# Optimization experiments

Hardware: AMD Instinct MI355X
Metric: run time of the kernel (lower is better)

## Reference

```python
import jax, jax.numpy as jnp
import numpy as np

RES = 32
HEADS = 16
EMB = 1024
DIM_HEAD = EMB // HEADS
BATCH = 8
N = RES * RES
SCALE = DIM_HEAD ** -0.5


def _make_bias_idxs():
    # replicate the LeViT-style |dx|,|dy| offset indexing from __init__
    points = [(i, j) for i in range(RES) for j in range(RES)]
    offsets = {}
    idxs = []
    for p1 in points:
        for p2 in points:
            off = (abs(p1[0] - p2[0]), abs(p1[1] - p2[1]))
            if off not in offsets:
                offsets[off] = len(offsets)
            idxs.append(offsets[off])
    return np.asarray(idxs, dtype=np.int32).reshape(N, N), len(offsets)


def setup_inputs() -> dict:
    key = jax.random.key(0)
    k_x, k_qkv, k_b, k_o = jax.random.split(key, 4)
    bias_idxs, n_off = _make_bias_idxs()  # n_off == 1024 for a 32x32 grid
    return {
        "x": jax.random.normal(k_x, (BATCH, N, EMB), dtype=jnp.float32),
        "W_qkv": jax.random.normal(k_qkv, (3 * EMB, EMB), dtype=jnp.float32) * 0.02,
        "attention_biases": jax.random.normal(k_b, (HEADS, n_off), dtype=jnp.float32) * 0.02,
        "bias_idxs": jnp.asarray(bias_idxs),
        "W_out": jax.random.normal(k_o, (EMB, EMB), dtype=jnp.float32) * 0.02,
        "b_out": jnp.zeros((EMB,), dtype=jnp.float32),
    }


def reference(x, W_qkv, attention_biases, bias_idxs, W_out, b_out):
    B, n, E = x.shape
    # to_qkv: Linear(E, 3E, bias=False) -> x @ W^T
    qkv = x @ W_qkv.T  # [B, n, 3E]
    q, k, v = jnp.split(qkv, 3, axis=-1)

    def heads(t):  # b n (h d) -> b h n d
        return t.reshape(B, n, HEADS, DIM_HEAD).transpose(0, 2, 1, 3)

    q, k, v = heads(q), heads(k), heads(v)
    qk = jnp.einsum("bhnd,bhmd->bhnm", q, k) * SCALE  # [B, h, n, n]
    bias = attention_biases[:, bias_idxs]  # gather -> [h, n, n]
    qk = qk + bias[None]
    attn = jax.nn.softmax(qk, axis=-1)
    out = jnp.einsum("bhnm,bhmd->bhnd", attn, v)
    out = out.transpose(0, 2, 1, 3).reshape(B, n, E)  # b h n d -> b n (h d)
    # to_out: Linear(E, E) with bias (dropout p=0 is identity)
    return out @ W_out.T + b_out
```

## Files before the change

### kernel.cpp

```cpp
#include <hip/hip_runtime.h>

typedef __attribute__((ext_vector_type(8))) short bf16x8;
typedef __attribute__((ext_vector_type(4))) short bf16x4;
typedef __attribute__((ext_vector_type(4))) float f32x4;

#define L2E 1.44269504088896340736f
#define QSCL 0.18033688011112042f

__device__ inline unsigned short f2bf(float f) {
  union { float f; unsigned int u; } x; x.f = f;
  return (unsigned short)((x.u + 0x8000u) >> 16);
}
__device__ inline unsigned int f2bf2(float a, float b) {
  union { float f; unsigned int u; } xa, xb;
  xa.f = a; xb.f = b;
  return ((xa.u + 0x8000u) >> 16) | (((xb.u + 0x8000u) & 0xFFFF0000u));
}
__device__ inline unsigned int pk_bf16(float a, float b) {
#if __has_builtin(__builtin_amdgcn_cvt_pk_bf16_f32)
  typedef __attribute__((ext_vector_type(2))) __bf16 bfv2;
  union { bfv2 v; unsigned int u; } x;
  x.v = __builtin_amdgcn_cvt_pk_bf16_f32(a, b);
  return x.u;
#else
  return f2bf2(a, b);
#endif
}

__device__ inline void gl_lds16(const void* g, void* l) {
  __builtin_amdgcn_global_load_lds((const __attribute__((address_space(1))) void*)g,
                                   (__attribute__((address_space(3))) void*)l,
                                   16, 0, 0);
}

__device__ inline void vm_drain() {
  asm volatile("s_waitcnt vmcnt(0)" ::: "memory");
}
__device__ inline void vm_wait4() {
  asm volatile("s_waitcnt vmcnt(4)" ::: "memory");
}
__device__ inline void vm_wait3() {
  asm volatile("s_waitcnt vmcnt(3)" ::: "memory");
}

#define N4_X  2097152
#define N4_WQ 786432
#define N4_WO 262144
__global__ void cast3_kernel(const float* __restrict__ x,
                             const float* __restrict__ wq,
                             const float* __restrict__ wo,
                             unsigned short* __restrict__ xb,
                             unsigned short* __restrict__ wqb,
                             unsigned short* __restrict__ wob) {
  int i = blockIdx.x * blockDim.x + threadIdx.x;
  int st = gridDim.x * blockDim.x;
  for (; i < N4_X + N4_WQ + N4_WO; i += st) {
    const float* src; unsigned short* dst; int j;
    if (i < N4_X)            { src = x;  dst = xb;  j = i; }
    else if (i < N4_X + N4_WQ){ src = wq; dst = wqb; j = i - N4_X; }
    else                     { src = wo; dst = wob; j = i - N4_X - N4_WQ; }
    float4 v = reinterpret_cast<const float4*>(src)[j];
    ushort4 o;
    o.x = f2bf(v.x); o.y = f2bf(v.y); o.z = f2bf(v.z); o.w = f2bf(v.w);
    reinterpret_cast<ushort4*>(dst)[j] = o;
  }
}

template <int MODE>
__device__ __forceinline__ void gemm_qkv_body(
    unsigned short* __restrict__ sA,
    unsigned short* __restrict__ sB,
    const unsigned short* __restrict__ A,
    const unsigned short* __restrict__ Bm,
    unsigned short* __restrict__ qo,
    unsigned short* __restrict__ ko,
    unsigned short* __restrict__ vo) {
  const int K = 1024;
  const int tid = threadIdx.x;
  const int w = tid >> 6, lane = tid & 63;
  const int l15 = lane & 15, quad = lane >> 4;
  const int wm = (w >> 1) * 64, wn = (w & 1) * 64;
  const int tm = blockIdx.y, tn = blockIdx.x;

  const unsigned short* Ab = A + (size_t)(tm * 128) * K;
  const unsigned short* Bb = Bm + (size_t)(tn * 128) * K;

  const int srow = w * 32 + (lane >> 2);
  const int scol = (((lane & 3) ^ ((lane >> 3) & 3))) * 8;
  const int rsw = (l15 >> 1) & 3;

  const f32x4 fz = {0.f, 0.f, 0.f, 0.f};
  f32x4 acc[4][4];
#pragma unroll
  for (int i = 0; i < 4; i++)
#pragma unroll
    for (int j = 0; j < 4; j++) acc[i][j] = fz;

#define QKV_STAGE(kn, nb)                                                        \
  do {                                                                           \
    gl_lds16(Ab + (size_t)srow * K + (kn) + scol,        &sA[(nb) * 4096 + (w * 32) * 32]);      \
    gl_lds16(Ab + (size_t)(srow + 16) * K + (kn) + scol, &sA[(nb) * 4096 + (w * 32 + 16) * 32]); \
    gl_lds16(Bb + (size_t)srow * K + (kn) + scol,        &sB[(nb) * 4096 + (w * 32) * 32]);      \
    gl_lds16(Bb + (size_t)(srow + 16) * K + (kn) + scol, &sB[(nb) * 4096 + (w * 32 + 16) * 32]); \
  } while (0)

  QKV_STAGE(0, 0);
  QKV_STAGE(32, 1);

  int bi = 0;
  for (int k0 = 0; k0 < K; k0 += 32) {
    if (k0 + 64 < K) vm_wait4(); else vm_drain();
    __syncthreads();
    if (k0 + 64 < K) {
      int nb = bi + 2; if (nb >= 3) nb -= 3;
      QKV_STAGE(k0 + 64, nb);
    }
    bf16x8 af[4], bfr[4];
#pragma unroll
    for (int mt = 0; mt < 4; mt++)
      af[mt] = *(const bf16x8*)&sA[bi * 4096 + (wm + mt * 16 + l15) * 32 + ((quad ^ rsw) << 3)];
#pragma unroll
    for (int nt = 0; nt < 4; nt++)
      bfr[nt] = *(const bf16x8*)&sB[bi * 4096 + (wn + nt * 16 + l15) * 32 + ((quad ^ rsw) << 3)];
#pragma unroll
    for (int mt = 0; mt < 4; mt++)
#pragma unroll
      for (int nt = 0; nt < 4; nt++) {
        if (MODE == 0)
          acc[mt][nt] = __builtin_amdgcn_mfma_f32_16x16x32_bf16(bfr[nt], af[mt], acc[mt][nt], 0, 0, 0);
        else
          acc[mt][nt] = __builtin_amdgcn_mfma_f32_16x16x32_bf16(af[mt], bfr[nt], acc[mt][nt], 0, 0, 0);
      }
    bi = bi + 1; if (bi == 3) bi = 0;
  }
#undef QKV_STAGE

  const int m0 = tm * 128;
  const int bb = m0 >> 10, n0 = m0 & 1023;
  const int cbase = (tn * 128) & 1023;

  if (MODE == 0) {
    const int which = tn >> 3;
    const float scl = (which == 0) ? QSCL : 1.0f;
    unsigned short* dst = (which == 0) ? qo : ko;
#pragma unroll
    for (int mt = 0; mt < 4; mt++) {
      int tok = n0 + wm + mt * 16 + l15;
#pragma unroll
      for (int nt = 0; nt < 4; nt++) {
        int c = cbase + wn + nt * 16 + quad * 4;
        int hh = c >> 6, d0 = c & 63;
        uint2 val;
        val.x = f2bf2(acc[mt][nt][0] * scl, acc[mt][nt][1] * scl);
        val.y = f2bf2(acc[mt][nt][2] * scl, acc[mt][nt][3] * scl);
        *(uint2*)&dst[(((size_t)bb * 16 + hh) * 1024 + tok) * 64 + d0] = val;
      }
    }
  } else {
#pragma unroll
    for (int mt = 0; mt < 4; mt++) {
      int tok = n0 + wm + mt * 16 + quad * 4;
#pragma unroll
      for (int nt = 0; nt < 4; nt++) {
        int c = cbase + wn + nt * 16 + l15;
        int hh = c >> 6, dd = c & 63;
        uint2 val;
        val.x = f2bf2(acc[mt][nt][0], acc[mt][nt][1]);
        val.y = f2bf2(acc[mt][nt][2], acc[mt][nt][3]);
        *(uint2*)&vo[(((size_t)bb * 16 + hh) * 64 + dd) * 1024 + tok] = val;
      }
    }
  }
}

__global__ __launch_bounds__(256, 3) void gemm_qkv(
    const unsigned short* __restrict__ A,
    const unsigned short* __restrict__ Bm,
    unsigned short* __restrict__ qo,
    unsigned short* __restrict__ ko,
    unsigned short* __restrict__ vo) {
  __shared__ unsigned short sA[3][128 * 32];
  __shared__ unsigned short sB[3][128 * 32];
  if (blockIdx.x < 16) gemm_qkv_body<0>(&sA[0][0], &sB[0][0], A, Bm, qo, ko, vo);
  else                 gemm_qkv_body<1>(&sA[0][0], &sB[0][0], A, Bm, qo, ko, vo);
}

__global__ __launch_bounds__(256, 2) void attn_kernel(
    const unsigned short* __restrict__ Q,
    const unsigned short* __restrict__ Kg,
    const unsigned short* __restrict__ Vt,
    const float* __restrict__ biases,
    unsigned short* __restrict__ Og) {
  __shared__ unsigned short sK[2][64 * 64];
  __shared__ unsigned short sV[2][64 * 64];
  __shared__ float sBias2[32 * 63];

  const int bx = blockIdx.x;
  const int bh = bx & 127, qt = bx >> 7;
  const int h = bh & 15, b = bh >> 4;
  const int tid = threadIdx.x, w = tid >> 6, lane = tid & 63;
  const int l15 = lane & 15, quad = lane >> 4;

  const size_t bhs = (size_t)(b * 16 + h);
  const unsigned short* qbase = Q + (bhs * 1024 + (size_t)qt * 256) * 64;
  const unsigned short* kbase = Kg + bhs * 1024 * 64;
  const unsigned short* vbase = Vt + bhs * 64 * 1024;

  for (int t = tid; t < 2048; t += 256) {
    int d = t >> 6, u = t & 63;
    if (u < 63) {
      int dj = u - 31; dj = dj < 0 ? -dj : dj;
      sBias2[d * 63 + u] = biases[h * 1024 + d * 32 + dj] * L2E;
    }
  }

  const int sr0 = w * 16 + (lane >> 3);
  const int sc8 = lane & 7;
  const int sw0 = sc8 ^ (lane >> 3);

  gl_lds16(kbase + (size_t)sr0 * 64 + sw0 * 8,        &sK[0][(w * 16) * 64]);
  gl_lds16(kbase + (size_t)(sr0 + 8) * 64 + sw0 * 8,  &sK[0][(w * 16 + 8) * 64]);
  gl_lds16(vbase + (size_t)sr0 * 1024 + sw0 * 8,      &sV[0][(w * 16) * 64]);
  gl_lds16(vbase + (size_t)(sr0 + 8) * 1024 + sw0 * 8,&sV[0][(w * 16 + 8) * 64]);

  bf16x8 qf[4][2];
#pragma unroll
  for (int qb = 0; qb < 4; qb++)
#pragma unroll
    for (int kd = 0; kd < 2; kd++)
      qf[qb][kd] = *(const bf16x8*)(qbase + (w * 64 + qb * 16 + l15) * 64 + kd * 32 + quad * 8);

  const int qg0 = qt * 256 + w * 64;
  const int qtw = __builtin_amdgcn_readfirstlane(qt * 8 + w * 2);
  int cc2[2][2];
#pragma unroll
  for (int qh = 0; qh < 2; qh++)
#pragma unroll
    for (int kp = 0; kp < 2; kp++)
      cc2[qh][kp] = qh * 16 + l15 - kp * 16 - quad * 4;

  const f32x4 fz = {0.f, 0.f, 0.f, 0.f};
  f32x4 of[4][4], osum[4];
#pragma unroll
  for (int i = 0; i < 4; i++) {
    osum[i] = fz;
#pragma unroll
    for (int j = 0; j < 4; j++) of[i][j] = fz;
  }
  const bf16x4 vones = {(short)0x3F80, (short)0x3F80, (short)0x3F80, (short)0x3F80};

  int buf = 0;
  for (int j0 = 0; j0 < 1024; j0 += 64) {
    vm_drain();
    __syncthreads();
    if (j0 + 64 < 1024) {
      int nb = buf ^ 1, jn = j0 + 64;
      gl_lds16(kbase + (size_t)(jn + sr0) * 64 + sw0 * 8,       &sK[nb][(w * 16) * 64]);
      gl_lds16(kbase + (size_t)(jn + sr0 + 8) * 64 + sw0 * 8,   &sK[nb][(w * 16 + 8) * 64]);
      gl_lds16(vbase + (size_t)sr0 * 1024 + jn + sw0 * 8,       &sV[nb][(w * 16) * 64]);
      gl_lds16(vbase + (size_t)(sr0 + 8) * 1024 + jn + sw0 * 8, &sV[nb][(w * 16 + 8) * 64]);
    }
    const unsigned short* K_ = sK[buf];
    const unsigned short* V_ = sV[buf];
    const int j5 = j0 >> 5;
    const int dh = qtw - j5;
    const float* b0 = sBias2 + abs(dh) * 63 + 31;
    const float* bM = sBias2 + abs(dh - 1) * 63 + 31;
    const float* bP = sBias2 + abs(dh + 1) * 63 + 31;

#pragma unroll
    for (int kvb = 0; kvb < 4; kvb++) {
      bf16x8 kf0 = *(const bf16x8*)&K_[(kvb * 16 + l15) * 64 + ((quad ^ (l15 & 7)) << 3)];
      bf16x8 kf1 = *(const bf16x8*)&K_[(kvb * 16 + l15) * 64 + (((4 + quad) ^ (l15 & 7)) << 3)];
      bf16x4 vf[4];
#pragma unroll
      for (int nt = 0; nt < 4; nt++) {
        int d = nt * 16 + l15;
        vf[nt] = *(const bf16x4*)&V_[d * 64 + (((kvb * 2 + (quad >> 1)) ^ (l15 & 7)) << 3) + (quad & 1) * 4];
      }
      const int kp = kvb & 1;
#pragma unroll
      for (int qb = 0; qb < 4; qb++) {
        f32x4 s4 = __builtin_amdgcn_mfma_f32_16x16x32_bf16(kf0, qf[qb][0], fz, 0, 0, 0);
        s4 = __builtin_amdgcn_mfma_f32_16x16x32_bf16(kf1, qf[qb][1], s4, 0, 0, 0);
        const float* bp = (qb < 2) ? ((kvb < 2) ? b0 : bM)
                                   : ((kvb < 2) ? bP : b0);
        const float* bq = bp + cc2[qb & 1][kp];
        float p0 = __builtin_amdgcn_exp2f(s4.x + bq[0]);
        float p1 = __builtin_amdgcn_exp2f(s4.y + bq[-1]);
        float p2 = __builtin_amdgcn_exp2f(s4.z + bq[-2]);
        float p3 = __builtin_amdgcn_exp2f(s4.w + bq[-3]);
        union { unsigned int u[2]; bf16x4 v; } pk;
        pk.u[0] = pk_bf16(p0, p1);
        pk.u[1] = pk_bf16(p2, p3);
#pragma unroll
        for (int nt = 0; nt < 4; nt++)
          of[qb][nt] = __builtin_amdgcn_mfma_f32_16x16x16bf16_1k(pk.v, vf[nt], of[qb][nt], 0, 0, 0);
        osum[qb] = __builtin_amdgcn_mfma_f32_16x16x16bf16_1k(pk.v, vones, osum[qb], 0, 0, 0);
      }
    }
    buf ^= 1;
  }

  const int kvq = quad * 4;
#pragma unroll
  for (int qb = 0; qb < 4; qb++)
#pragma unroll
    for (int r = 0; r < 4; r++) {
      float inv = __builtin_amdgcn_rcpf(osum[qb][r]);
      int n = qg0 + qb * 16 + kvq + r;
      size_t orow = ((size_t)b * 1024 + n) * 1024 + h * 64;
#pragma unroll
      for (int nt = 0; nt < 4; nt++)
        Og[orow + nt * 16 + l15] = f2bf(of[qb][nt][r] * inv);
    }
}

__global__ __launch_bounds__(256, 4) void gemm_out_k(
    const unsigned short* __restrict__ A,
    const unsigned short* __restrict__ Bm,
    const float* __restrict__ bias,
    float* __restrict__ out) {
  __shared__ unsigned short sA[3][128 * 32];
  __shared__ unsigned short sB[3][64 * 32];
  const int K = 1024;
  const int tid = threadIdx.x;
  const int w = tid >> 6, lane = tid & 63;
  const int l15 = lane & 15, quad = lane >> 4;
  const int tm = blockIdx.y, tn = blockIdx.x;

  const unsigned short* Ab = A + (size_t)(tm * 128) * K;
  const unsigned short* Bb = Bm + (size_t)(tn * 64) * K;

  const int srowA = w * 32 + (lane >> 2);
  const int srowB = w * 16 + (lane >> 2);
  const int scol = (((lane & 3) ^ ((lane >> 3) & 3))) * 8;
  const int rsw = (l15 >> 1) & 3;

  const f32x4 fz = {0.f, 0.f, 0.f, 0.f};
  f32x4 acc[2][4];
#pragma unroll
  for (int i = 0; i < 2; i++)
#pragma unroll
    for (int j = 0; j < 4; j++) acc[i][j] = fz;

#define OUT_STAGE(kn, nb)                                                          \
  do {                                                                             \
    gl_lds16(Ab + (size_t)srowA * K + (kn) + scol,        &sA[nb][(w * 32) * 32]);      \
    gl_lds16(Ab + (size_t)(srowA + 16) * K + (kn) + scol, &sA[nb][(w * 32 + 16) * 32]); \
    gl_lds16(Bb + (size_t)srowB * K + (kn) + scol,        &sB[nb][(w * 16) * 32]);      \
  } while (0)

  OUT_STAGE(0, 0);
  OUT_STAGE(32, 1);

  int bi = 0;
  for (int k0 = 0; k0 < K; k0 += 32) {
    if (k0 + 64 < K) vm_wait3(); else vm_drain();
    __syncthreads();
    if (k0 + 64 < K) {
      int nb = bi + 2; if (nb >= 3) nb -= 3;
      OUT_STAGE(k0 + 64, nb);
    }
    bf16x8 af[2], bfr[4];
#pragma unroll
    for (int mt = 0; mt < 2; mt++)
      af[mt] = *(const bf16x8*)&sA[bi][(w * 32 + mt * 16 + l15) * 32 + ((quad ^ rsw) << 3)];
#pragma unroll
    for (int nt = 0; nt < 4; nt++)
      bfr[nt] = *(const bf16x8*)&sB[bi][(nt * 16 + l15) * 32 + ((quad ^ rsw) << 3)];
#pragma unroll
    for (int mt = 0; mt < 2; mt++)
#pragma unroll
      for (int nt = 0; nt < 4; nt++)
        acc[mt][nt] = __builtin_amdgcn_mfma_f32_16x16x32_bf16(af[mt], bfr[nt], acc[mt][nt], 0, 0, 0);
    bi = bi + 1; if (bi == 3) bi = 0;
  }
#undef OUT_STAGE

  const int m0 = tm * 128 + w * 32, c0 = tn * 64;
#pragma unroll
  for (int mt = 0; mt < 2; mt++)
#pragma unroll
    for (int nt = 0; nt < 4; nt++)
#pragma unroll
      for (int r = 0; r < 4; r++) {
        int m = m0 + mt * 16 + quad * 4 + r;
        int c = c0 + nt * 16 + l15;
        out[(size_t)m * 1024 + c] = acc[mt][nt][r] + bias[c];
      }
}

extern "C" void kernel_launch(void* const* d_in, const int* in_sizes, int n_in,
                              void* d_out, int out_size, void* d_ws, size_t ws_size,
                              hipStream_t stream) {
  const float* x    = (const float*)d_in[0];
  const float* Wqkv = (const float*)d_in[1];
  const float* ab   = (const float*)d_in[2];
  const float* Wout = (const float*)d_in[4];
  const float* bout = (const float*)d_in[5];
  float* out = (float*)d_out;

  char* ws = (char*)d_ws;
  unsigned short* xb  = (unsigned short*)(ws);
  unsigned short* wqb = (unsigned short*)(ws + 16777216);
  unsigned short* wob = (unsigned short*)(ws + 23068672);
  unsigned short* qw  = (unsigned short*)(ws + 25165824);
  unsigned short* kw  = (unsigned short*)(ws + 41943040);
  unsigned short* vw  = (unsigned short*)(ws + 58720256);
  unsigned short* ow  = (unsigned short*)(ws + 75497472);

  cast3_kernel<<<1536, 256, 0, stream>>>(x, Wqkv, Wout, xb, wqb, wob);
  gemm_qkv<<<dim3(24, 64), 256, 0, stream>>>(xb, wqb, qw, kw, vw);
  attn_kernel<<<512, 256, 0, stream>>>(qw, kw, vw, ab, ow);
  gemm_out_k<<<dim3(16, 64), 256, 0, stream>>>(ow, wob, bout, out);
}
```

Baseline: 258.1 us.

## Rewrite QKV GEMM with 256x256 tiles, 8 waves, and ping-pong staged loads

The QKV projection GEMM moves from 128x128 tiles with 4 waves and a 3-stage K=32 pipeline to 256x256 tiles with 8 waves and K=64 double buffering. Global-to-LDS loads for the next tile are split into quarters and interleaved between four MFMA phases, with s_setprio raised around the math. The grid becomes 1D and is remapped so consecutive blocks are spread across XCDs. The aim is better operand reuse and overlap of loads with MFMA work. In exchange it uses 128KB of LDS per block, many more accumulator registers, and more barriers per K step.

```diff
diff --git a/kernel.cpp b/kernel.cpp
--- a/kernel.cpp
+++ b/kernel.cpp
@@ -67,88 +67,162 @@
 }
 
 template <int MODE>
-__device__ __forceinline__ void gemm_qkv_body(
-    unsigned short* __restrict__ sA,
-    unsigned short* __restrict__ sB,
+__device__ __forceinline__ void qkv_body(
+    unsigned short* lds,
     const unsigned short* __restrict__ A,
     const unsigned short* __restrict__ Bm,
     unsigned short* __restrict__ qo,
     unsigned short* __restrict__ ko,
-    unsigned short* __restrict__ vo) {
-  const int K = 1024;
+    unsigned short* __restrict__ vo,
+    int tm, int tn) {
   const int tid = threadIdx.x;
   const int w = tid >> 6, lane = tid & 63;
   const int l15 = lane & 15, quad = lane >> 4;
-  const int wm = (w >> 1) * 64, wn = (w & 1) * 64;
-  const int tm = blockIdx.y, tn = blockIdx.x;
-
-  const unsigned short* Ab = A + (size_t)(tm * 128) * K;
-  const unsigned short* Bb = Bm + (size_t)(tn * 128) * K;
-
-  const int srow = w * 32 + (lane >> 2);
-  const int scol = (((lane & 3) ^ ((lane >> 3) & 3))) * 8;
-  const int rsw = (l15 >> 1) & 3;
+  const int wmb = (w >> 2) * 128;
+  const int wnb = (w & 3) * 64;
+  const int rl = (w << 3) + (lane >> 3);
+  const int scol = ((lane & 7) ^ ((lane >> 3) & 7)) << 3;
+  const int rk = l15 & 7;
+
+  const unsigned short* Ab = A + (size_t)(tm * 256) * 1024;
+  const unsigned short* Bb = Bm + (size_t)(tn * 256) * 1024;
+
+  unsigned short* sA0 = lds;
+  unsigned short* sA1 = lds + 16384;
+  unsigned short* sB0 = lds + 32768;
+  unsigned short* sB1 = lds + 49152;
+
+#define STG_HALF(Gb, R0, k0, Lb)                                              \
+  do {                                                                        \
+    gl_lds16((Gb) + (size_t)((R0) + rl) * 1024 + (k0) + scol,                 \
+             (Lb) + ((R0) + (w << 3)) * 64);                                  \
+    gl_lds16((Gb) + (size_t)((R0) + 64 + rl) * 1024 + (k0) + scol,            \
+             (Lb) + ((R0) + 64 + (w << 3)) * 64);                             \
+  } while (0)
+
+#define LDF(buf, row, kk) \
+  (*(const bf16x8*)&(buf)[(row) * 64 + ((((kk) * 4 + quad) ^ rk) << 3)])
+
+  STG_HALF(Ab, 0, 0, sA0);
+  STG_HALF(Ab, 128, 0, sA0);
+  STG_HALF(Bb, 0, 0, sB0);
+  STG_HALF(Bb, 128, 0, sB0);
+  STG_HALF(Bb, 0, 64, sB1);
+  STG_HALF(Bb, 128, 64, sB1);
 
   const f32x4 fz = {0.f, 0.f, 0.f, 0.f};
-  f32x4 acc[4][4];
-#pragma unroll
-  for (int i = 0; i < 4; i++)
+  f32x4 acc[8][4];
+#pragma unroll
+  for (int i = 0; i < 8; i++)
 #pragma unroll
     for (int j = 0; j < 4; j++) acc[i][j] = fz;
 
-#define QKV_STAGE(kn, nb)                                                        \
-  do {                                                                           \
-    gl_lds16(Ab + (size_t)srow * K + (kn) + scol,        &sA[(nb) * 4096 + (w * 32) * 32]);      \
-    gl_lds16(Ab + (size_t)(srow + 16) * K + (kn) + scol, &sA[(nb) * 4096 + (w * 32 + 16) * 32]); \
-    gl_lds16(Bb + (size_t)srow * K + (kn) + scol,        &sB[(nb) * 4096 + (w * 32) * 32]);      \
-    gl_lds16(Bb + (size_t)(srow + 16) * K + (kn) + scol, &sB[(nb) * 4096 + (w * 32 + 16) * 32]); \
-  } while (0)
-
-  QKV_STAGE(0, 0);
-  QKV_STAGE(32, 1);
-
-  int bi = 0;
-  for (int k0 = 0; k0 < K; k0 += 32) {
-    if (k0 + 64 < K) vm_wait4(); else vm_drain();
-    __syncthreads();
-    if (k0 + 64 < K) {
-      int nb = bi + 2; if (nb >= 3) nb -= 3;
-      QKV_STAGE(k0 + 64, nb);
-    }
-    bf16x8 af[4], bfr[4];
-#pragma unroll
-    for (int mt = 0; mt < 4; mt++)
-      af[mt] = *(const bf16x8*)&sA[bi * 4096 + (wm + mt * 16 + l15) * 32 + ((quad ^ rsw) << 3)];
-#pragma unroll
-    for (int nt = 0; nt < 4; nt++)
-      bfr[nt] = *(const bf16x8*)&sB[bi * 4096 + (wn + nt * 16 + l15) * 32 + ((quad ^ rsw) << 3)];
-#pragma unroll
-    for (int mt = 0; mt < 4; mt++)
+  vm_wait4();
+  __syncthreads();
+
+  for (int t = 0; t < 16; ++t) {
+    unsigned short* Ac = (t & 1) ? sA1 : sA0;
+    unsigned short* An = (t & 1) ? sA0 : sA1;
+    unsigned short* Bc = (t & 1) ? sB1 : sB0;
+    bf16x8 a0[4][2], a1[4][2], b0[2][2], b1[2][2];
+
+#pragma unroll
+    for (int mt = 0; mt < 4; mt++)
+#pragma unroll
+      for (int kk = 0; kk < 2; kk++)
+        a0[mt][kk] = LDF(Ac, wmb + mt * 16 + l15, kk);
+#pragma unroll
+    for (int nt = 0; nt < 2; nt++)
+#pragma unroll
+      for (int kk = 0; kk < 2; kk++)
+        b0[nt][kk] = LDF(Bc, wnb + nt * 16 + l15, kk);
+    if (t < 15) STG_HALF(Ab, 0, (t + 1) << 6, An);
+    __syncthreads();
+    __builtin_amdgcn_s_setprio(1);
+#pragma unroll
+    for (int mt = 0; mt < 4; mt++)
+#pragma unroll
+      for (int nt = 0; nt < 2; nt++)
+#pragma unroll
+        for (int kk = 0; kk < 2; kk++)
+          acc[mt][nt] = (MODE == 0)
+            ? __builtin_amdgcn_mfma_f32_16x16x32_bf16(b0[nt][kk], a0[mt][kk], acc[mt][nt], 0, 0, 0)
+            : __builtin_amdgcn_mfma_f32_16x16x32_bf16(a0[mt][kk], b0[nt][kk], acc[mt][nt], 0, 0, 0);
+    __builtin_amdgcn_s_setprio(0);
+    __syncthreads();
+
+#pragma unroll
+    for (int nt = 0; nt < 2; nt++)
+#pragma unroll
+      for (int kk = 0; kk < 2; kk++)
+        b1[nt][kk] = LDF(Bc, wnb + (nt + 2) * 16 + l15, kk);
+    if (t < 15) STG_HALF(Ab, 128, (t + 1) << 6, An);
+    __syncthreads();
+    __builtin_amdgcn_s_setprio(1);
+#pragma unroll
+    for (int mt = 0; mt < 4; mt++)
+#pragma unroll
+      for (int nt = 0; nt < 2; nt++)
+#pragma unroll
+        for (int kk = 0; kk < 2; kk++)
+          acc[mt][nt + 2] = (MODE == 0)
+            ? __builtin_amdgcn_mfma_f32_16x16x32_bf16(b1[nt][kk], a0[mt][kk], acc[mt][nt + 2], 0, 0, 0)
+            : __builtin_amdgcn_mfma_f32_16x16x32_bf16(a0[mt][kk], b1[nt][kk], acc[mt][nt + 2], 0, 0, 0);
+    __builtin_amdgcn_s_setprio(0);
+    __syncthreads();
+
+#pragma unroll
+    for (int mt = 0; mt < 4; mt++)
+#pragma unroll
+      for (int kk = 0; kk < 2; kk++)
+        a1[mt][kk] = LDF(Ac, wmb + (mt + 4) * 16 + l15, kk);
+    if (t < 14) STG_HALF(Bb, 0, (t + 2) << 6, Bc);
+    __syncthreads();
+    __builtin_amdgcn_s_setprio(1);
+#pragma unroll
+    for (int mt = 0; mt < 4; mt++)
+#pragma unroll
+      for (int nt = 0; nt < 2; nt++)
+#pragma unroll
+        for (int kk = 0; kk < 2; kk++)
+          acc[mt + 4][nt] = (MODE == 0)
+            ? __builtin_amdgcn_mfma_f32_16x16x32_bf16(b0[nt][kk], a1[mt][kk], acc[mt + 4][nt], 0, 0, 0)
+            : __builtin_amdgcn_mfma_f32_16x16x32_bf16(a1[mt][kk], b0[nt][kk], acc[mt + 4][nt], 0, 0, 0);
+    __builtin_amdgcn_s_setprio(0);
+    __syncthreads();
+
+    if (t < 14) STG_HALF(Bb, 128, (t + 2) << 6, Bc);
+    __syncthreads();
+    __builtin_amdgcn_s_setprio(1);
+#pragma unroll
+    for (int mt = 0; mt < 4; mt++)
+#pragma unroll
+      for (int nt = 0; nt < 2; nt++)
+#pragma unroll
+        for (int kk = 0; kk < 2; kk++)
+          acc[mt + 4][nt + 2] = (MODE == 0)
+            ? __builtin_amdgcn_mfma_f32_16x16x32_bf16(b1[nt][kk], a1[mt][kk], acc[mt + 4][nt + 2], 0, 0, 0)
+            : __builtin_amdgcn_mfma_f32_16x16x32_bf16(a1[mt][kk], b1[nt][kk], acc[mt + 4][nt + 2], 0, 0, 0);
+    __builtin_amdgcn_s_setprio(0);
+    if (t < 14) vm_wait4();
+    else if (t == 14) vm_drain();
+    __syncthreads();
+  }
+#undef STG_HALF
+#undef LDF
+
+  const int bb = tm >> 2;
+  const int n0 = (tm & 3) << 8;
+  const int cb = (tn & 3) << 8;
+  if (MODE == 0) {
+    const float scl = (tn < 4) ? QSCL : 1.0f;
+    unsigned short* dst = (tn < 4) ? qo : ko;
+#pragma unroll
+    for (int mt = 0; mt < 8; mt++) {
+      int tok = n0 + wmb + mt * 16 + l15;
 #pragma unroll
       for (int nt = 0; nt < 4; nt++) {
-        if (MODE == 0)
-          acc[mt][nt] = __builtin_amdgcn_mfma_f32_16x16x32_bf16(bfr[nt], af[mt], acc[mt][nt], 0, 0, 0);
-        else
-          acc[mt][nt] = __builtin_amdgcn_mfma_f32_16x16x32_bf16(af[mt], bfr[nt], acc[mt][nt], 0, 0, 0);
-      }
-    bi = bi + 1; if (bi == 3) bi = 0;
-  }
-#undef QKV_STAGE
-
-  const int m0 = tm * 128;
-  const int bb = m0 >> 10, n0 = m0 & 1023;
-  const int cbase = (tn * 128) & 1023;
-
-  if (MODE == 0) {
-    const int which = tn >> 3;
-    const float scl = (which == 0) ? QSCL : 1.0f;
-    unsigned short* dst = (which == 0) ? qo : ko;
-#pragma unroll
-    for (int mt = 0; mt < 4; mt++) {
-      int tok = n0 + wm + mt * 16 + l15;
-#pragma unroll
-      for (int nt = 0; nt < 4; nt++) {
-        int c = cbase + wn + nt * 16 + quad * 4;
+        int c = cb + wnb + nt * 16 + quad * 4;
         int hh = c >> 6, d0 = c & 63;
         uint2 val;
         val.x = f2bf2(acc[mt][nt][0] * scl, acc[mt][nt][1] * scl);
@@ -158,11 +232,11 @@
     }
   } else {
 #pragma unroll
-    for (int mt = 0; mt < 4; mt++) {
-      int tok = n0 + wm + mt * 16 + quad * 4;
+    for (int mt = 0; mt < 8; mt++) {
+      int tok = n0 + wmb + mt * 16 + quad * 4;
 #pragma unroll
       for (int nt = 0; nt < 4; nt++) {
-        int c = cbase + wn + nt * 16 + l15;
+        int c = cb + wnb + nt * 16 + l15;
         int hh = c >> 6, dd = c & 63;
         uint2 val;
         val.x = f2bf2(acc[mt][nt][0], acc[mt][nt][1]);
@@ -173,16 +247,18 @@
   }
 }
 
-__global__ __launch_bounds__(256, 3) void gemm_qkv(
+__global__ __launch_bounds__(512, 2) void gemm_qkv(
     const unsigned short* __restrict__ A,
     const unsigned short* __restrict__ Bm,
     unsigned short* __restrict__ qo,
     unsigned short* __restrict__ ko,
     unsigned short* __restrict__ vo) {
-  __shared__ unsigned short sA[3][128 * 32];
-  __shared__ unsigned short sB[3][128 * 32];
-  if (blockIdx.x < 16) gemm_qkv_body<0>(&sA[0][0], &sB[0][0], A, Bm, qo, ko, vo);
-  else                 gemm_qkv_body<1>(&sA[0][0], &sB[0][0], A, Bm, qo, ko, vo);
+  __shared__ unsigned short lds[65536];
+  const int id = blockIdx.x;
+  const int wg = (id & 7) * 48 + (id >> 3);
+  const int tm = wg / 12, tn = wg - tm * 12;
+  if (tn < 8) qkv_body<0>(lds, A, Bm, qo, ko, vo, tm, tn);
+  else        qkv_body<1>(lds, A, Bm, qo, ko, vo, tm, tn);
 }
 
 __global__ __launch_bounds__(256, 2) void attn_kernel(
@@ -411,7 +487,7 @@
   unsigned short* ow  = (unsigned short*)(ws + 75497472);
 
   cast3_kernel<<<1536, 256, 0, stream>>>(x, Wqkv, Wout, xb, wqb, wob);
-  gemm_qkv<<<dim3(24, 64), 256, 0, stream>>>(xb, wqb, qw, kw, vw);
+  gemm_qkv<<<384, 512, 0, stream>>>(xb, wqb, qw, kw, vw);
   attn_kernel<<<512, 256, 0, stream>>>(qw, kw, vw, ab, ow);
   gemm_out_k<<<dim3(16, 64), 256, 0, stream>>>(ow, wob, bout, out);
 }
```

New measurement: 289.9 us. 12.3% more time.
